# Performance work log

Hardware: AMD Instinct MI355X
Metric: run time of the kernel (lower is better)

The kernel has to match this reference:

```python
import jax, jax.numpy as jnp
import numpy as np

M0 = 0.3  # DTM mass parameter (layer init m0)
LIMS = [[-1.0, 1.0], [-1.0, 1.0]]
BY = 0.025


def _make_grid(lims, by):
    # Exact replica of tf_gridBy (including row ordering via full transpose)
    axes = [np.arange(lo, hi + by, by, dtype=np.float32) for lo, hi in lims]
    mesh = np.stack(np.meshgrid(*axes, indexing='ij'), 0)   # [d, n1, n2]
    grid = np.transpose(mesh).reshape(-1, len(lims))        # [N, d]
    return jnp.asarray(grid)


def setup_inputs() -> dict:
    key = jax.random.key(0)
    k1, k2 = jax.random.split(key)
    B, M = 2, 2048
    inputs = jax.random.normal(k1, (B, M, 2), dtype=jnp.float32)
    weight = jax.random.uniform(k2, (B, M), dtype=jnp.float32)  # positive weights
    grid = _make_grid(LIMS, BY)  # [6561, 2]
    return {"inputs": inputs, "weight": weight, "grid": grid}


def reference(inputs, weight, grid):
    # inputs: [B, M, d], weight: [B, M], grid: [N, d] -> dtm: [B, N]
    # Uses k = M (full sorted neighbor list); identical math to the original
    # data-dependent k = max(searchsorted)+1 truncation, since searchsorted
    # selects the same prefix index either way.
    wB = M0 * jnp.sum(weight, -1, keepdims=True)            # [B, 1] weightBound

    # Brute-force euclidean cdist grid -> points (tf_knn, r=2)
    X2 = jnp.sum(inputs * inputs, -1)                        # [B, M]
    G2 = jnp.sum(grid * grid, -1)                            # [N]
    XG = jnp.einsum('bmd,nd->bnm', inputs, grid)             # [B, N, M]
    dist = jnp.sqrt(jnp.maximum(G2[None, :, None] + X2[:, None, :] - 2.0 * XG, 0.0))

    # Full ascending sort = top_k with k=M (knnDistance, knnIndex)
    idx = jnp.argsort(dist, axis=-1)                         # [B, N, M]
    dsort = jnp.take_along_axis(dist, idx, axis=-1)

    # gather weights by neighbor index, cumulative mass
    wTemp = jnp.take_along_axis(jnp.broadcast_to(weight[:, None, :], idx.shape), idx, axis=-1)
    wcum = jnp.cumsum(wTemp, -1)                             # [B, N, M]

    bound = wB[..., None]                                    # [B, 1, 1]
    # searchsorted(side='left') == count of entries strictly below bound
    kidx = jnp.sum(wcum < bound, -1)                         # [B, N]

    d2 = dsort * dsort
    cumD = jnp.cumsum(d2 * wTemp, -1)
    val = cumD + d2 * (bound - wcum)                         # [B, N, M]
    sel = jnp.take_along_axis(val, kidx[..., None], axis=-1)[..., 0]  # [B, N]
    return jnp.sqrt(sel / wB)
```

## Files before the change

### kernel.cpp

```cpp
#include <hip/hip_runtime.h>
#include <math.h>


#define M_POINTS 2048
#define PER_LANE 32
#define M0 0.3f

__device__ __forceinline__ float wave_reduce_sum(float v) {
    #pragma unroll
    for (int off = 1; off < 64; off <<= 1)
        v += __shfl_xor(v, off, 64);
    return v;
}
__device__ __forceinline__ float wave_reduce_max(float v) {
    #pragma unroll
    for (int off = 1; off < 64; off <<= 1)
        v = fmaxf(v, __shfl_xor(v, off, 64));
    return v;
}
__device__ __forceinline__ float wave_reduce_min(float v) {
    #pragma unroll
    for (int off = 1; off < 64; off <<= 1)
        v = fminf(v, __shfl_xor(v, off, 64));
    return v;
}

__global__ __launch_bounds__(256) void dtm_kernel(
    const float* __restrict__ inputs,
    const float* __restrict__ weight,
    const float* __restrict__ grid,
    float* __restrict__ out,
    int B, int N)
{
    const int lane = threadIdx.x & 63;
    const int gwave = blockIdx.x * (blockDim.x >> 6) + (threadIdx.x >> 6);
    if (gwave >= B * N) return;
    const int b = gwave / N;
    const int n = gwave - b * N;

    const float gx = grid[2 * n];
    const float gy = grid[2 * n + 1];

    const float* __restrict__ inb = inputs + (size_t)b * M_POINTS * 2;
    const float* __restrict__ wb  = weight + (size_t)b * M_POINTS;

    const int base = lane * PER_LANE;
    const float4* __restrict__ xyv = reinterpret_cast<const float4*>(inb + 2 * base);
    const float4* __restrict__ wv  = reinterpret_cast<const float4*>(wb + base);

    float d2[PER_LANE], w[PER_LANE];
    float wsum_local = 0.0f, vmax_local = 0.0f;
    #pragma unroll
    for (int q = 0; q < PER_LANE / 4; ++q) {
        const float4 wq = wv[q];
        const float4 a  = xyv[2 * q];
        const float4 c4 = xyv[2 * q + 1];
        float dx, dy;
        dx = a.x  - gx; dy = a.y  - gy; d2[4*q+0] = fmaf(dx, dx, dy * dy);
        dx = a.z  - gx; dy = a.w  - gy; d2[4*q+1] = fmaf(dx, dx, dy * dy);
        dx = c4.x - gx; dy = c4.y - gy; d2[4*q+2] = fmaf(dx, dx, dy * dy);
        dx = c4.z - gx; dy = c4.w - gy; d2[4*q+3] = fmaf(dx, dx, dy * dy);
        w[4*q+0] = wq.x; w[4*q+1] = wq.y; w[4*q+2] = wq.z; w[4*q+3] = wq.w;
        wsum_local += wq.x + wq.y + wq.z + wq.w;
        vmax_local = fmaxf(vmax_local, fmaxf(fmaxf(d2[4*q+0], d2[4*q+1]),
                                             fmaxf(d2[4*q+2], d2[4*q+3])));
    }
    const float total = wave_reduce_sum(wsum_local);
    const float bound = M0 * total;

    float vlo = -1.0f, wlo = 0.0f;
    float vhi = wave_reduce_max(vmax_local), whi = total;
    #pragma unroll 1
    for (int it = 0; it < 48; ++it) {
        if (whi - wlo <= 0.75f) break;
        const float vmid = 0.5f * (vlo + vhi);
        if (!(vmid > vlo && vmid < vhi)) break;
        float c = 0.0f;
        #pragma unroll
        for (int j = 0; j < PER_LANE; ++j)
            c += (d2[j] <= vmid) ? w[j] : 0.0f;
        c = wave_reduce_sum(c);
        if (c >= bound) { vhi = vmid; whi = c; }
        else            { vlo = vmid; wlo = c; }
    }

    float r2 = vhi, W = wlo;
    #pragma unroll 1
    for (int step = 0; step < 64; ++step) {
        float m = __builtin_inff();
        #pragma unroll
        for (int j = 0; j < PER_LANE; ++j)
            m = fminf(m, (d2[j] > vlo) ? d2[j] : __builtin_inff());
        m = wave_reduce_min(m);
        float c = 0.0f;
        #pragma unroll
        for (int j = 0; j < PER_LANE; ++j)
            c += (d2[j] <= m) ? w[j] : 0.0f;
        c = wave_reduce_sum(c);
        if (c >= bound) { r2 = m; W = wlo; break; }
        vlo = m; wlo = c;
    }

    float S = 0.0f;
    #pragma unroll
    for (int j = 0; j < PER_LANE; ++j)
        if (d2[j] < r2) S = fmaf(w[j], d2[j], S);
    S = wave_reduce_sum(S);

    const float margin = fmaxf(bound - W, 0.0f);
    const float val = fmaxf(fmaf(r2, margin, S), 0.0f);
    if (lane == 0) out[gwave] = sqrtf(val / bound);
}

extern "C" void kernel_launch(void* const* d_in, const int* in_sizes, int n_in,
                              void* d_out, int out_size, void* d_ws, size_t ws_size,
                              hipStream_t stream) {
    const float* inputs = (const float*)d_in[0];
    const float* weight = (const float*)d_in[1];
    const float* grid   = (const float*)d_in[2];
    float* out = (float*)d_out;

    const int N = in_sizes[2] / 2;
    const int B = out_size / N;

    const int total_waves = B * N;
    const int waves_per_block = 256 / 64;
    const int blocks = (total_waves + waves_per_block - 1) / waves_per_block;

    dtm_kernel<<<blocks, 256, 0, stream>>>(inputs, weight, grid, out, B, N);
}
```

Baseline: 128.2 us.

## Process two grid points per wavefront to share point loads and interleave reductions

Each wavefront now handles two adjacent grid points for the same batch. It loads the point coordinates and weights once and computes two distance arrays, then runs both bisection and refinement searches in lockstep so their independent shuffle reductions can overlap. The final partial mass W is now recomputed as a masked sum rather than carried from the search. This adds register pressure (96 floats per lane) and halves the number of waves, which could lower occupancy, and one point may iterate longer than it needs while waiting for the other.

Result: slower. 169.7 us (+32.3%).

```diff
diff --git a/kernel.cpp b/kernel.cpp
--- a/kernel.cpp
+++ b/kernel.cpp
@@ -33,13 +33,17 @@
     int B, int N)
 {
     const int lane = threadIdx.x & 63;
-    const int gwave = blockIdx.x * (blockDim.x >> 6) + (threadIdx.x >> 6);
-    if (gwave >= B * N) return;
-    const int b = gwave / N;
-    const int n = gwave - b * N;
+    const int task = blockIdx.x * (blockDim.x >> 6) + (threadIdx.x >> 6);
+    const int halfN = (N + 1) >> 1;
+    if (task >= B * halfN) return;
+    const int b  = task / halfN;
+    const int r  = task - b * halfN;
+    const int n0 = 2 * r;
+    const bool has1 = (n0 + 1 < N);
+    const int n1 = has1 ? n0 + 1 : n0;
 
-    const float gx = grid[2 * n];
-    const float gy = grid[2 * n + 1];
+    const float gxa = grid[2 * n0], gya = grid[2 * n0 + 1];
+    const float gxb = grid[2 * n1], gyb = grid[2 * n1 + 1];
 
     const float* __restrict__ inb = inputs + (size_t)b * M_POINTS * 2;
     const float* __restrict__ wb  = weight + (size_t)b * M_POINTS;
@@ -48,68 +52,97 @@
     const float4* __restrict__ xyv = reinterpret_cast<const float4*>(inb + 2 * base);
     const float4* __restrict__ wv  = reinterpret_cast<const float4*>(wb + base);
 
-    float d2[PER_LANE], w[PER_LANE];
-    float wsum_local = 0.0f, vmax_local = 0.0f;
+    float d2a[PER_LANE], d2b[PER_LANE], w[PER_LANE];
+    float wsum_local = 0.0f, vmaxa_l = 0.0f, vmaxb_l = 0.0f;
     #pragma unroll
     for (int q = 0; q < PER_LANE / 4; ++q) {
         const float4 wq = wv[q];
-        const float4 a  = xyv[2 * q];
-        const float4 c4 = xyv[2 * q + 1];
-        float dx, dy;
-        dx = a.x  - gx; dy = a.y  - gy; d2[4*q+0] = fmaf(dx, dx, dy * dy);
-        dx = a.z  - gx; dy = a.w  - gy; d2[4*q+1] = fmaf(dx, dx, dy * dy);
-        dx = c4.x - gx; dy = c4.y - gy; d2[4*q+2] = fmaf(dx, dx, dy * dy);
-        dx = c4.z - gx; dy = c4.w - gy; d2[4*q+3] = fmaf(dx, dx, dy * dy);
-        w[4*q+0] = wq.x; w[4*q+1] = wq.y; w[4*q+2] = wq.z; w[4*q+3] = wq.w;
-        wsum_local += wq.x + wq.y + wq.z + wq.w;
-        vmax_local = fmaxf(vmax_local, fmaxf(fmaxf(d2[4*q+0], d2[4*q+1]),
-                                             fmaxf(d2[4*q+2], d2[4*q+3])));
+        const float4 p0 = xyv[2 * q];
+        const float4 p1 = xyv[2 * q + 1];
+        const float xs[4] = {p0.x, p0.z, p1.x, p1.z};
+        const float ys[4] = {p0.y, p0.w, p1.y, p1.w};
+        const float ws4[4] = {wq.x, wq.y, wq.z, wq.w};
+        #pragma unroll
+        for (int t = 0; t < 4; ++t) {
+            const int j = 4 * q + t;
+            float dx = xs[t] - gxa, dy = ys[t] - gya;
+            d2a[j] = fmaf(dx, dx, dy * dy);
+            dx = xs[t] - gxb; dy = ys[t] - gyb;
+            d2b[j] = fmaf(dx, dx, dy * dy);
+            w[j] = ws4[t];
+            wsum_local += ws4[t];
+            vmaxa_l = fmaxf(vmaxa_l, d2a[j]);
+            vmaxb_l = fmaxf(vmaxb_l, d2b[j]);
+        }
     }
     const float total = wave_reduce_sum(wsum_local);
     const float bound = M0 * total;
 
-    float vlo = -1.0f, wlo = 0.0f;
-    float vhi = wave_reduce_max(vmax_local), whi = total;
+    float vloA = 0.0f, wloA = 0.0f, vhiA = wave_reduce_max(vmaxa_l), whiA = total;
+    float vloB = 0.0f, wloB = 0.0f, vhiB = wave_reduce_max(vmaxb_l), whiB = total;
     #pragma unroll 1
     for (int it = 0; it < 48; ++it) {
-        if (whi - wlo <= 0.75f) break;
-        const float vmid = 0.5f * (vlo + vhi);
-        if (!(vmid > vlo && vmid < vhi)) break;
-        float c = 0.0f;
+        const float vmA = 0.5f * (vloA + vhiA);
+        const float vmB = 0.5f * (vloB + vhiB);
+        const bool actA = (whiA - wloA > 0.75f) && (vmA > vloA) && (vmA < vhiA);
+        const bool actB = (whiB - wloB > 0.75f) && (vmB > vloB) && (vmB < vhiB);
+        if (!actA && !actB) break;
+        float cA = 0.0f, cB = 0.0f;
         #pragma unroll
-        for (int j = 0; j < PER_LANE; ++j)
-            c += (d2[j] <= vmid) ? w[j] : 0.0f;
-        c = wave_reduce_sum(c);
-        if (c >= bound) { vhi = vmid; whi = c; }
-        else            { vlo = vmid; wlo = c; }
+        for (int j = 0; j < PER_LANE; ++j) {
+            cA += (d2a[j] <= vmA) ? w[j] : 0.0f;
+            cB += (d2b[j] <= vmB) ? w[j] : 0.0f;
+        }
+        cA = wave_reduce_sum(cA);
+        cB = wave_reduce_sum(cB);
+        if (actA) { if (cA >= bound) { vhiA = vmA; whiA = cA; }
+                    else             { vloA = vmA; wloA = cA; } }
+        if (actB) { if (cB >= bound) { vhiB = vmB; whiB = cB; }
+                    else             { vloB = vmB; wloB = cB; } }
     }
 
-    float r2 = vhi, W = wlo;
+    float r2A = vhiA, r2B = vhiB;
+    bool foundA = false, foundB = false;
     #pragma unroll 1
     for (int step = 0; step < 64; ++step) {
-        float m = __builtin_inff();
+        if (foundA && foundB) break;
+        float mA = __builtin_inff(), mB = __builtin_inff();
         #pragma unroll
-        for (int j = 0; j < PER_LANE; ++j)
-            m = fminf(m, (d2[j] > vlo) ? d2[j] : __builtin_inff());
-        m = wave_reduce_min(m);
-        float c = 0.0f;
+        for (int j = 0; j < PER_LANE; ++j) {
+            mA = fminf(mA, (d2a[j] > vloA) ? d2a[j] : __builtin_inff());
+            mB = fminf(mB, (d2b[j] > vloB) ? d2b[j] : __builtin_inff());
+        }
+        mA = wave_reduce_min(mA);
+        mB = wave_reduce_min(mB);
+        float cA = 0.0f, cB = 0.0f;
         #pragma unroll
-        for (int j = 0; j < PER_LANE; ++j)
-            c += (d2[j] <= m) ? w[j] : 0.0f;
-        c = wave_reduce_sum(c);
-        if (c >= bound) { r2 = m; W = wlo; break; }
-        vlo = m; wlo = c;
+        for (int j = 0; j < PER_LANE; ++j) {
+            cA += (d2a[j] <= mA) ? w[j] : 0.0f;
+            cB += (d2b[j] <= mB) ? w[j] : 0.0f;
+        }
+        cA = wave_reduce_sum(cA);
+        cB = wave_reduce_sum(cB);
+        if (!foundA) { if (cA >= bound) { r2A = mA; foundA = true; } else vloA = mA; }
+        if (!foundB) { if (cB >= bound) { r2B = mB; foundB = true; } else vloB = mB; }
     }
 
-    float S = 0.0f;
+    float SA = 0.0f, WA = 0.0f, SB = 0.0f, WB = 0.0f;
     #pragma unroll
-    for (int j = 0; j < PER_LANE; ++j)
-        if (d2[j] < r2) S = fmaf(w[j], d2[j], S);
-    S = wave_reduce_sum(S);
+    for (int j = 0; j < PER_LANE; ++j) {
+        if (d2a[j] < r2A) { SA = fmaf(w[j], d2a[j], SA); WA += w[j]; }
+        if (d2b[j] < r2B) { SB = fmaf(w[j], d2b[j], SB); WB += w[j]; }
+    }
+    SA = wave_reduce_sum(SA); WA = wave_reduce_sum(WA);
+    SB = wave_reduce_sum(SB); WB = wave_reduce_sum(WB);
 
-    const float margin = fmaxf(bound - W, 0.0f);
-    const float val = fmaxf(fmaf(r2, margin, S), 0.0f);
-    if (lane == 0) out[gwave] = sqrtf(val / bound);
+    if (lane == 0) {
+        const float valA = fmaxf(fmaf(r2A, fmaxf(bound - WA, 0.0f), SA), 0.0f);
+        out[(size_t)b * N + n0] = sqrtf(valA / bound);
+        if (has1) {
+            const float valB = fmaxf(fmaf(r2B, fmaxf(bound - WB, 0.0f), SB), 0.0f);
+            out[(size_t)b * N + n0 + 1] = sqrtf(valB / bound);
+        }
+    }
 }
 
 extern "C" void kernel_launch(void* const* d_in, const int* in_sizes, int n_in,
@@ -122,10 +155,11 @@
 
     const int N = in_sizes[2] / 2;
     const int B = out_size / N;
+    const int halfN = (N + 1) >> 1;
+    const int total_tasks = B * halfN;
 
-    const int total_waves = B * N;
     const int waves_per_block = 256 / 64;
-    const int blocks = (total_waves + waves_per_block - 1) / waves_per_block;
+    const int blocks = (total_tasks + waves_per_block - 1) / waves_per_block;
 
     dtm_kernel<<<blocks, 256, 0, stream>>>(inputs, weight, grid, out, B, N);
 }
```
